# Optimization experiments

Hardware: AMD Instinct MI355X
Metric: run time of the kernel (lower is better)

Reference implementation:

```python
import jax, jax.numpy as jnp
import numpy as np
from jax import lax

CANTOR_DEPTH = 8
VOCAB, D = 100000, 128


def setup_inputs() -> dict:
    key = jax.random.key(0)
    pentachora = jax.random.normal(key, (VOCAB, 5, D), dtype=jnp.float32)
    return {"pentachora": pentachora}


def _cantor_positions(V):
    # V: [N, 5, D]
    dt = V.dtype
    diff = V[:, :, None, :] - V[:, None, :, :]          # [N,5,5,D]
    dist_sq = jnp.sum(diff * diff, axis=-1)             # [N,5,5]
    N = V.shape[0]

    # Batched 6x6 Cayley-Menger matrix
    M = jnp.zeros((N, 6, 6), dtype=dt)
    M = M.at[:, 0, 1:].set(1.0)
    M = M.at[:, 1:, 0].set(1.0)
    M = M.at[:, 1:, 1:].set(dist_sq)
    det = jnp.linalg.det(M)                              # [N]
    volume = jnp.sqrt(jnp.clip(-det / 9216.0, 0.0))

    # Edge statistics over the 10 unique edges (torch .std() uses ddof=1)
    iu, ju = np.triu_indices(5, k=1)
    edge_lengths = jnp.sqrt(dist_sq[:, iu, ju])          # [N,10]
    mean_edge = jnp.mean(edge_lengths, axis=-1)
    std_edge = jnp.std(edge_lengths, axis=-1, ddof=1)

    # Vertex spread from centroid (ddof=1)
    centroid = jnp.mean(V, axis=1, keepdims=True)        # [N,1,D]
    cdist = jnp.linalg.norm(V - centroid, axis=-1)       # [N,5]
    spread = jnp.std(cdist, axis=-1, ddof=1)

    volume_norm = jax.nn.sigmoid(volume * 10.0)
    edge_ratio = jax.nn.sigmoid(std_edge / (mean_edge + 1e-6))
    spread_norm = jax.nn.sigmoid(spread)

    seed = jnp.clip(volume_norm * 0.4 + edge_ratio * 0.3 + spread_norm * 0.3,
                    1e-6, 1.0 - 1e-6)
    drift = (volume_norm + edge_ratio + spread_norm) * 0.01

    def step(carry, factor):
        x, cv = carry
        x_scaled = x * 3.0
        digit = jnp.floor(x_scaled)                      # x>0 so floor==trunc
        x_frac = x_scaled - digit
        cv = cv + (digit == 2.0).astype(dt) * factor
        x = jnp.clip(x_frac + drift, 1e-6, 1.0 - 1e-6)
        return (x, cv), None

    factors = (0.5 ** jnp.arange(1, CANTOR_DEPTH + 1)).astype(dt)
    (_, cantor_val), _ = lax.scan(step, (seed, jnp.zeros_like(seed)), factors)
    return jnp.clip(cantor_val, 0.0, 1.0)                # [N]


def reference(pentachora):
    return _cantor_positions(pentachora)
```

## Files before the change

kernel.cpp:

```cpp
#include <hip/hip_runtime.h>
#include <math.h>


__global__ __launch_bounds__(256) void fingerprint_kernel(
    const float* __restrict__ pent, float* __restrict__ out, int nItems)
{
    const int tid  = threadIdx.x;
    const int wave = tid >> 6;
    const int lane = tid & 63;
    const int grp  = lane >> 3;
    const int s    = lane & 7;

    long item  = (long)blockIdx.x * 32 + (long)wave * 8 + grp;
    long itemC = item < nItems ? item : (long)nItems - 1;

    const float4* __restrict__ p =
        reinterpret_cast<const float4*>(pent + itemC * 640L);

    float4 f[5][4];
#pragma unroll
    for (int v = 0; v < 5; ++v)
#pragma unroll
        for (int j = 0; j < 4; ++j)
            f[v][j] = p[v * 32 + j * 8 + s];

    const float* fp = reinterpret_cast<const float*>(f);

    double sp[10];
    double sc[5];
#pragma unroll
    for (int q = 0; q < 10; ++q) sp[q] = 0.0;
#pragma unroll
    for (int v = 0; v < 5; ++v)  sc[v] = 0.0;

#pragma unroll
    for (int t = 0; t < 16; ++t) {
        double a[5];
#pragma unroll
        for (int v = 0; v < 5; ++v)
            a[v] = (double)fp[v * 16 + t];
        int q = 0;
#pragma unroll
        for (int i = 0; i < 5; ++i)
#pragma unroll
            for (int j = i + 1; j < 5; ++j) {
                double d = a[i] - a[j];
                sp[q] = fma(d, d, sp[q]);
                ++q;
            }
        double c = (a[0] + a[1] + a[2] + a[3] + a[4]) * 0.2;
#pragma unroll
        for (int v = 0; v < 5; ++v) {
            double d = a[v] - c;
            sc[v] = fma(d, d, sc[v]);
        }
    }

#pragma unroll
    for (int m = 1; m <= 4; m <<= 1) {
#pragma unroll
        for (int q = 0; q < 10; ++q) sp[q] += __shfl_xor(sp[q], m, 64);
#pragma unroll
        for (int v = 0; v < 5; ++v)  sc[v] += __shfl_xor(sc[v], m, 64);
    }


    double A[6][6];
    A[0][0] = 1.0; A[0][1] = 0.0;
    A[1][0] = 0.0; A[1][1] = 1.0;
#pragma unroll
    for (int j = 2; j < 6; ++j) { A[1][j] = 1.0; }
#pragma unroll
    for (int i = 2; i < 6; ++i) { A[i][0] = 1.0; A[i][i] = 0.0; }
    {
        int q = 0;
#pragma unroll
        for (int i = 0; i < 5; ++i)
#pragma unroll
            for (int j = i + 1; j < 5; ++j) {
                int ri = (i == 0) ? 0 : (1 + i);
                int rj = (j == 0) ? 0 : (1 + j);
                A[ri][1 + j] = sp[q];
                A[rj][1 + i] = sp[q];
                ++q;
            }
    }

    double det = -1.0;
#pragma unroll
    for (int k = 0; k < 6; ++k) {
        double pv = A[k][k];
        det *= pv;
        double inv = (pv != 0.0) ? 1.0 / pv : 0.0;
#pragma unroll
        for (int r = k + 1; r < 6; ++r) {
            double fac = A[r][k] * inv;
#pragma unroll
            for (int c = k + 1; c < 6; ++c)
                A[r][c] = fma(-fac, A[k][c], A[r][c]);
        }
    }

    double v2 = -det / 9216.0;
    double volume = (v2 > 0.0) ? sqrt(v2) : 0.0;

    double e[10], se = 0.0;
#pragma unroll
    for (int q = 0; q < 10; ++q) { e[q] = sqrt(sp[q]); se += e[q]; }
    double meanE = se * 0.1;
    double ve = 0.0;
#pragma unroll
    for (int q = 0; q < 10; ++q) { double d = e[q] - meanE; ve = fma(d, d, ve); }
    double stdE = sqrt(ve / 9.0);

    double cd[5], scd = 0.0;
#pragma unroll
    for (int v = 0; v < 5; ++v) { cd[v] = sqrt(sc[v]); scd += cd[v]; }
    double meanC = scd * 0.2;
    double vc = 0.0;
#pragma unroll
    for (int v = 0; v < 5; ++v) { double d = cd[v] - meanC; vc = fma(d, d, vc); }
    double spread = sqrt(vc * 0.25);

    double vn = 1.0 / (1.0 + exp(-10.0 * volume));
    double er = 1.0 / (1.0 + exp(-(stdE / (meanE + 1e-6))));
    double sn = 1.0 / (1.0 + exp(-spread));

    double seed = 0.4 * vn + 0.3 * er + 0.3 * sn;
    seed = fmin(fmax(seed, 1e-6), 1.0 - 1e-6);
    double drift = (vn + er + sn) * 0.01;

    double x = seed, cv = 0.0, factor = 0.5;
#pragma unroll
    for (int k = 0; k < 8; ++k) {
        double xs = x * 3.0;
        double dg = floor(xs);
        double fr = xs - dg;
        cv += (dg == 2.0) ? factor : 0.0;
        factor *= 0.5;
        x = fmin(fmax(fr + drift, 1e-6), 1.0 - 1e-6);
    }
    cv = fmin(fmax(cv, 0.0), 1.0);

    if (s == 0 && item < nItems)
        out[item] = (float)cv;
}

extern "C" void kernel_launch(void* const* d_in, const int* in_sizes, int n_in,
                              void* d_out, int out_size, void* d_ws, size_t ws_size,
                              hipStream_t stream) {
    const float* pent = (const float*)d_in[0];
    float* out = (float*)d_out;
    int nItems = in_sizes[0] / 640;
    int blocks = (nItems + 31) / 32;
    hipLaunchKernelGGL(fingerprint_kernel, dim3(blocks), dim3(256), 0, stream,
                       pent, out, nItems);
}
```

Before: 51.43 us.

## Derive distances, centroid spread and volume from a single Gram matrix

Each item now accumulates one 15-entry Gram matrix of vertex dot products instead of 10 pairwise squared distances plus 5 centroid distances. Edge lengths and centroid distances are then computed algebraically from it, and the volume comes from a 4x4 edge Gram determinant in place of the 6x6 Cayley-Menger elimination. This lowers the double-precision FMA count in the inner loop and shortens the elimination. The cost is possible cancellation when distances are formed from large dot products, which can perturb the floor-based Cantor digits.

```diff
diff --git a/kernel.cpp b/kernel.cpp
--- a/kernel.cpp
+++ b/kernel.cpp
@@ -26,12 +26,9 @@
 
     const float* fp = reinterpret_cast<const float*>(f);
 
-    double sp[10];
-    double sc[5];
+    double g[15];
 #pragma unroll
-    for (int q = 0; q < 10; ++q) sp[q] = 0.0;
-#pragma unroll
-    for (int v = 0; v < 5; ++v)  sc[v] = 0.0;
+    for (int q = 0; q < 15; ++q) g[q] = 0.0;
 
 #pragma unroll
     for (int t = 0; t < 16; ++t) {
@@ -43,70 +40,78 @@
 #pragma unroll
         for (int i = 0; i < 5; ++i)
 #pragma unroll
-            for (int j = i + 1; j < 5; ++j) {
-                double d = a[i] - a[j];
-                sp[q] = fma(d, d, sp[q]);
+            for (int j = i; j < 5; ++j) {
+                g[q] = fma(a[i], a[j], g[q]);
                 ++q;
             }
-        double c = (a[0] + a[1] + a[2] + a[3] + a[4]) * 0.2;
-#pragma unroll
-        for (int v = 0; v < 5; ++v) {
-            double d = a[v] - c;
-            sc[v] = fma(d, d, sc[v]);
-        }
     }
 
 #pragma unroll
-    for (int m = 1; m <= 4; m <<= 1) {
+    for (int m = 1; m <= 4; m <<= 1)
 #pragma unroll
-        for (int q = 0; q < 10; ++q) sp[q] += __shfl_xor(sp[q], m, 64);
+        for (int q = 0; q < 15; ++q) g[q] += __shfl_xor(g[q], m, 64);
+
+
+    double G[5][5];
+    {
+        int q = 0;
 #pragma unroll
-        for (int v = 0; v < 5; ++v)  sc[v] += __shfl_xor(sc[v], m, 64);
+        for (int i = 0; i < 5; ++i)
+#pragma unroll
+            for (int j = i; j < 5; ++j) {
+                G[i][j] = g[q];
+                G[j][i] = g[q];
+                ++q;
+            }
     }
 
+    double S[5], T = 0.0;
+#pragma unroll
+    for (int i = 0; i < 5; ++i) {
+        S[i] = G[i][0] + G[i][1] + G[i][2] + G[i][3] + G[i][4];
+        T += S[i];
+    }
 
-    double A[6][6];
-    A[0][0] = 1.0; A[0][1] = 0.0;
-    A[1][0] = 0.0; A[1][1] = 1.0;
-#pragma unroll
-    for (int j = 2; j < 6; ++j) { A[1][j] = 1.0; }
-#pragma unroll
-    for (int i = 2; i < 6; ++i) { A[i][0] = 1.0; A[i][i] = 0.0; }
+    double d2[10];
     {
         int q = 0;
 #pragma unroll
         for (int i = 0; i < 5; ++i)
 #pragma unroll
             for (int j = i + 1; j < 5; ++j) {
-                int ri = (i == 0) ? 0 : (1 + i);
-                int rj = (j == 0) ? 0 : (1 + j);
-                A[ri][1 + j] = sp[q];
-                A[rj][1 + i] = sp[q];
+                d2[q] = fma(-2.0, G[i][j], G[i][i] + G[j][j]);
                 ++q;
             }
     }
 
-    double det = -1.0;
+    double W[4][4];
 #pragma unroll
-    for (int k = 0; k < 6; ++k) {
-        double pv = A[k][k];
+    for (int pi = 0; pi < 4; ++pi)
+#pragma unroll
+        for (int qi = 0; qi < 4; ++qi)
+            W[pi][qi] = G[pi + 1][qi + 1] - G[0][qi + 1] - G[pi + 1][0] + G[0][0];
+
+    double det = 1.0;
+#pragma unroll
+    for (int k = 0; k < 4; ++k) {
+        double pv = W[k][k];
         det *= pv;
         double inv = (pv != 0.0) ? 1.0 / pv : 0.0;
 #pragma unroll
-        for (int r = k + 1; r < 6; ++r) {
-            double fac = A[r][k] * inv;
+        for (int r = k + 1; r < 4; ++r) {
+            double fac = W[r][k] * inv;
 #pragma unroll
-            for (int c = k + 1; c < 6; ++c)
-                A[r][c] = fma(-fac, A[k][c], A[r][c]);
+            for (int c = k + 1; c < 4; ++c)
+                W[r][c] = fma(-fac, W[k][c], W[r][c]);
         }
     }
 
-    double v2 = -det / 9216.0;
+    double v2 = det / 576.0;
     double volume = (v2 > 0.0) ? sqrt(v2) : 0.0;
 
     double e[10], se = 0.0;
 #pragma unroll
-    for (int q = 0; q < 10; ++q) { e[q] = sqrt(sp[q]); se += e[q]; }
+    for (int q = 0; q < 10; ++q) { e[q] = sqrt(d2[q]); se += e[q]; }
     double meanE = se * 0.1;
     double ve = 0.0;
 #pragma unroll
@@ -115,7 +120,11 @@
 
     double cd[5], scd = 0.0;
 #pragma unroll
-    for (int v = 0; v < 5; ++v) { cd[v] = sqrt(sc[v]); scd += cd[v]; }
+    for (int v = 0; v < 5; ++v) {
+        double c2 = fma(-0.4, S[v], G[v][v]) + 0.04 * T;
+        cd[v] = (c2 > 0.0) ? sqrt(c2) : 0.0;
+        scd += cd[v];
+    }
     double meanC = scd * 0.2;
     double vc = 0.0;
 #pragma unroll
```

Measured after the change: 49.36 us. -4.0%, faster.
